# Performance work log

Hardware: AMD Instinct MI355X
Metric: run time of the kernel (lower is better)

The kernel has to match this reference:

```python
import jax, jax.numpy as jnp
import numpy as np

IMAGE_W, IMAGE_H = 1024, 800
STRIDES = (8, 16, 32, 64, 128)
LEVEL_HW = ((100, 128), (50, 64), (25, 32), (13, 16), (7, 8))
TOP_N = 1000
MIN_SCORE = 0.01
NMS_THR = 0.6
MAX_DET = 100
NUM_CLASSES = 80
BATCH = 16


def _grid(h, w, stride, b):
    ys = (jnp.arange(h, dtype=jnp.float32) + 0.5) * stride
    xs = (jnp.arange(w, dtype=jnp.float32) + 0.5) * stride
    gx, gy = jnp.meshgrid(xs, ys)  # [h, w]
    pos = jnp.stack([gx, gy], axis=-1)  # [h, w, 2] = (x, y)
    return jnp.broadcast_to(pos, (b, h, w, 2))


def setup_inputs() -> dict:
    key = jax.random.key(0)
    inp = {}
    for i, ((h, w), s) in enumerate(zip(LEVEL_HW, STRIDES)):
        key, k1, k2, k3 = jax.random.split(key, 4)
        inp[f"cls{i}"] = jax.random.normal(k1, (BATCH, h, w, NUM_CLASSES), jnp.float32)
        # +3 so exp(reg) gives realistic ~20px box extents
        inp[f"reg{i}"] = jax.random.normal(k2, (BATCH, h, w, 4), jnp.float32) + 3.0
        inp[f"ctr{i}"] = jax.random.normal(k3, (BATCH, h, w, 1), jnp.float32)
        inp[f"pos{i}"] = _grid(h, w, s, BATCH)
    return inp


def _level_filter(cls, reg, ctr, pos):
    b = cls.shape[0]
    cls = jax.nn.sigmoid(cls).reshape(b, -1, NUM_CLASSES)
    reg = jnp.exp(reg).reshape(b, -1, 4)
    ctr = jax.nn.sigmoid(ctr).reshape(b, -1)
    pos = pos.reshape(b, -1, 2)
    scores = jnp.sqrt(jnp.max(cls, axis=2) * ctr)  # [b, n]
    classes = jnp.argmax(cls, axis=2)  # [b, n] int
    if scores.shape[1] >= TOP_N:
        scores, idx = jax.lax.top_k(scores, TOP_N)
        classes = jnp.take_along_axis(classes, idx, axis=1)
        reg = jnp.take_along_axis(reg, idx[..., None], axis=1)
        pos = jnp.take_along_axis(pos, idx[..., None], axis=1)
        cls = jnp.take_along_axis(cls, idx[..., None], axis=1)
    return scores, classes, reg, pos, cls


def _decode_boxes(reg, pos):
    # ltrb offsets -> x1y1x2y2, truncate to int (torch .int()), clamp to image
    xy_min = pos - reg[..., 0:2]
    xy_max = pos + reg[..., 2:4]
    bx = jnp.trunc(jnp.concatenate([xy_min, xy_max], axis=-1))
    x1 = jnp.maximum(bx[..., 0], 0.0)
    y1 = jnp.maximum(bx[..., 1], 0.0)
    x2 = jnp.minimum(bx[..., 2], IMAGE_W - 1.0)
    y2 = jnp.minimum(bx[..., 3], IMAGE_H - 1.0)
    return jnp.stack([x1, y1, x2, y2], axis=-1)


def _nms_image(scores, classes, boxes, clsp):
    valid = scores > MIN_SCORE
    order = jnp.argsort(jnp.where(valid, -scores, jnp.inf))  # valid, desc score first
    s = scores[order]
    c = classes[order].astype(jnp.float32)
    b = boxes[order]
    cp = clsp[order]
    v = valid[order]
    # pairwise IoU (keep/suppress decisions are not differentiated)
    bb = jax.lax.stop_gradient(b)
    area = (bb[:, 2] - bb[:, 0]) * (bb[:, 3] - bb[:, 1])
    lt = jnp.maximum(bb[:, None, :2], bb[None, :, :2])
    rb = jnp.minimum(bb[:, None, 2:], bb[None, :, 2:])
    wh = jnp.maximum(rb - lt, 0.0)
    inter = wh[..., 0] * wh[..., 1]
    iou = inter / (area[:, None] + area[None, :] - inter)
    n = s.shape[0]
    idxs = jnp.arange(n)

    def body(i, keep):
        sup = keep[i] & (iou[i] > NMS_THR) & (idxs > i)
        return keep & ~sup

    keep = jax.lax.fori_loop(0, n, body, v)
    rank = jnp.cumsum(keep) - 1
    slot = jnp.where(keep & (rank < MAX_DET), rank, MAX_DET)  # MAX_DET -> dropped
    out_s = jnp.full((MAX_DET,), -1.0, jnp.float32).at[slot].set(s, mode="drop")
    out_c = jnp.full((MAX_DET,), -1.0, jnp.float32).at[slot].set(c, mode="drop")
    out_b = jnp.full((MAX_DET, 4), -1.0, jnp.float32).at[slot].set(b, mode="drop")
    out_cp = jnp.full((MAX_DET, NUM_CLASSES), -1.0, jnp.float32).at[slot].set(cp, mode="drop")
    return out_s, out_c, out_b, out_cp


def reference(cls0, cls1, cls2, cls3, cls4, reg0, reg1, reg2, reg3, reg4,
              ctr0, ctr1, ctr2, ctr3, ctr4, pos0, pos1, pos2, pos3, pos4):
    clss = [cls0, cls1, cls2, cls3, cls4]
    regs = [reg0, reg1, reg2, reg3, reg4]
    ctrs = [ctr0, ctr1, ctr2, ctr3, ctr4]
    poss = [pos0, pos1, pos2, pos3, pos4]
    parts = [_level_filter(c, r, t, p) for c, r, t, p in zip(clss, regs, ctrs, poss)]
    scores = jnp.concatenate([p[0] for p in parts], axis=1)
    classes = jnp.concatenate([p[1] for p in parts], axis=1)
    reg = jnp.concatenate([p[2] for p in parts], axis=1)
    pos = jnp.concatenate([p[3] for p in parts], axis=1)
    clsp = jnp.concatenate([p[4] for p in parts], axis=1)
    boxes = _decode_boxes(reg, pos)
    return jax.vmap(_nms_image)(scores, classes, boxes, clsp)
```

## Files before the change

### kernel.cpp

```cpp
#include <hip/hip_runtime.h>
#include <math.h>

#define TOTAL_G 17064
#define BATCHN  16
#define ALLF    0xFFFFFFFFFFFFFFFFull
#define INVALID_HI 0xC3DC28F5u

typedef unsigned long long u64;
typedef unsigned int u32;
typedef unsigned short u16;

#define KEYS0_OFF   0
#define KEYS1_OFF   1638400
#define KEYS234_OFF 2048000
#define CLSI_OFF    2187264
#define NC_OFF      2733312
#define T512_OFF    2733824
#define KR_OFF      2733952
#define MSK_OFF     2799488
#define SLOTK_OFF   3323776

struct Ptrs {
  const float *cls0,*cls1,*cls2,*cls3,*cls4;
  const float *reg0,*reg1,*reg2,*reg3,*reg4;
  const float *ctr0,*ctr1,*ctr2,*ctr3,*ctr4;
  const float *pos0,*pos1,*pos2,*pos3,*pos4;
  char *ws;
};

__device__ __forceinline__ float sigd(float x) {
  return (float)(1.0 / (1.0 + exp(-(double)x)));
}
__device__ __forceinline__ float dexp(float x) {
  return (float)exp((double)x);
}
__device__ __forceinline__ void levinfo(int gid, int& lev, int& idx, int& nl) {
  if      (gid < 12800) { lev=0; idx=gid;        nl=12800; }
  else if (gid < 16000) { lev=1; idx=gid-12800;  nl=3200;  }
  else if (gid < 16800) { lev=2; idx=gid-16000;  nl=800;   }
  else if (gid < 17008) { lev=3; idx=gid-16800;  nl=208;   }
  else                  { lev=4; idx=gid-17008;  nl=56;    }
}

__device__ __forceinline__ u64* krank_of(char* ws, int b) {
  return (u64*)(ws + KR_OFF + (size_t)b * 4096);
}
__device__ __forceinline__ u64* msk_of(char* ws, int b) {
  return (u64*)(ws + MSK_OFF + (size_t)b * 32768);
}
__device__ __forceinline__ u64* slotkey_of(char* ws, int b) {
  return (u64*)(ws + SLOTK_OFF + (size_t)b * 800);
}

__device__ __forceinline__ float4 decode_box(const Ptrs& P, int b, int gid) {
  int lev, idx, nl; levinfo(gid, lev, idx, nl);
  const float *rp, *pp;
  if      (lev == 0) { rp = P.reg0; pp = P.pos0; }
  else if (lev == 1) { rp = P.reg1; pp = P.pos1; }
  else if (lev == 2) { rp = P.reg2; pp = P.pos2; }
  else if (lev == 3) { rp = P.reg3; pp = P.pos3; }
  else               { rp = P.reg4; pp = P.pos4; }
  float4 rv = *(const float4*)(rp + (size_t)(b * nl + idx) * 4);
  float2 pv = *(const float2*)(pp + (size_t)(b * nl + idx) * 2);
  float e0 = dexp(rv.x), e1 = dexp(rv.y), e2 = dexp(rv.z), e3 = dexp(rv.w);
  float x1 = truncf(pv.x - e0), y1 = truncf(pv.y - e1);
  float x2 = truncf(pv.x + e2), y2 = truncf(pv.y + e3);
  x1 = fmaxf(x1, 0.0f); y1 = fmaxf(y1, 0.0f);
  x2 = fminf(x2, 1023.0f); y2 = fminf(y2, 799.0f);
  return make_float4(x1, y1, x2, y2);
}

__global__ __launch_bounds__(256) void k_score(Ptrs P) {
  __shared__ float4 sk4[64 * 20];
  int b = blockIdx.y;
  int tid = threadIdx.x;
  int p0 = blockIdx.x * 64;

  #pragma unroll
  for (int it = 0; it < 5; ++it) {
    int t4 = it * 256 + tid;
    int g = p0 + t4 / 20;
    if (g < TOTAL_G) {
      int sub = t4 - (t4 / 20) * 20;
      int lev, idx, nl; levinfo(g, lev, idx, nl);
      const float* clsb;
      if      (lev == 0) clsb = P.cls0;
      else if (lev == 1) clsb = P.cls1;
      else if (lev == 2) clsb = P.cls2;
      else if (lev == 3) clsb = P.cls3;
      else               clsb = P.cls4;
      sk4[t4] = ((const float4*)(clsb + (size_t)(b * nl + idx) * 80))[sub];
    }
  }
  __syncthreads();

  int lp = tid >> 2, q = tid & 3;
  int g = p0 + lp;
  if (g >= TOTAL_G) return;

  const float4* my4 = &sk4[lp * 20 + q * 5];
  float m = -INFINITY, m2 = -INFINITY; int mi = 0;
  #pragma unroll
  for (int k = 0; k < 5; ++k) {
    float4 v = my4[k];
    int base = q * 20 + 4 * k;
    if (v.x > m) { m2 = m; m = v.x; mi = base+0; } else if (v.x > m2) m2 = v.x;
    if (v.y > m) { m2 = m; m = v.y; mi = base+1; } else if (v.y > m2) m2 = v.y;
    if (v.z > m) { m2 = m; m = v.z; mi = base+2; } else if (v.z > m2) m2 = v.z;
    if (v.w > m) { m2 = m; m = v.w; mi = base+3; } else if (v.w > m2) m2 = v.w;
  }
  #pragma unroll
  for (int xw = 1; xw <= 2; xw <<= 1) {
    float om  = __shfl_xor(m,  xw);
    float om2 = __shfl_xor(m2, xw);
    int   omi = __shfl_xor(mi, xw);
    bool take = (om > m) || (om == m && omi < mi);
    float lm  = take ? m : om;
    float wm2 = take ? om2 : m2;
    if (take) { m = om; mi = omi; }
    m2 = fmaxf(lm, wm2);
  }

  float thr = fminf(m - 1e-3f, 9.0f);
  float pmax; int ci;
  if (m2 >= thr) {
    float pv = -1.0f; int pi = 0x7fffffff;
    #pragma unroll 1
    for (int k = 0; k < 5; ++k) {
      float4 v = my4[k];
      float xs[4] = {v.x, v.y, v.z, v.w};
      #pragma unroll
      for (int e = 0; e < 4; ++e) {
        if (xs[e] >= thr) {
          float p = sigd(xs[e]);
          if (p > pv) { pv = p; pi = q * 20 + 4 * k + e; }
        }
      }
    }
    #pragma unroll
    for (int xw = 1; xw <= 2; xw <<= 1) {
      float ov = __shfl_xor(pv, xw);
      int   oi = __shfl_xor(pi, xw);
      if (ov > pv || (ov == pv && oi < pi)) { pv = ov; pi = oi; }
    }
    pmax = pv; ci = pi;
  } else {
    pmax = sigd(m); ci = mi;
  }

  if (q == 0) {
    int lev, idx, nl; levinfo(g, lev, idx, nl);
    const float* ctrb;
    if      (lev == 0) ctrb = P.ctr0;
    else if (lev == 1) ctrb = P.ctr1;
    else if (lev == 2) ctrb = P.ctr2;
    else if (lev == 3) ctrb = P.ctr3;
    else               ctrb = P.ctr4;
    float tc = ctrb[(size_t)b * nl + idx];
    float csig = sigd(tc);
    float prod = pmax * csig;
    float s = (float)sqrt((double)prod);
    ((u16*)(P.ws + CLSI_OFF))[(size_t)b * TOTAL_G + g] = (u16)ci;
    unsigned hi = ~__float_as_uint(s);
    u64 key = ((u64)hi << 15) | (unsigned)g;
    if      (lev == 0) ((u64*)(P.ws + KEYS0_OFF))  [(size_t)b * 12800 + idx] = key;
    else if (lev == 1) ((u64*)(P.ws + KEYS1_OFF))  [(size_t)b * 3200  + idx] = key;
    else               ((u64*)(P.ws + KEYS234_OFF))[(size_t)b * 1088  + (g - 16000)] = key;
  }
}

struct SelSh {
  u32 hist[4][4096];
  u64 buf[64];
  u64 res, pfx;
  int t, mode, cnt;
};

__device__ __forceinline__ u64 loadkey(const Ptrs& P, int b, int u) {
  if (u < 12800) return ((const u64*)(P.ws + KEYS0_OFF))  [(size_t)b * 12800 + u];
  if (u < 16000) return ((const u64*)(P.ws + KEYS1_OFF))  [(size_t)b * 3200  + (u - 12800)];
  return               ((const u64*)(P.ws + KEYS234_OFF))[(size_t)b * 1088  + (u - 16000)];
}
__device__ __forceinline__ bool keep_pred(u64 k, int u, u64 T0, u64 T1) {
  bool valid = (u32)(k >> 15) < INVALID_HI;
  bool sel = (u < 12800) ? (k <= T0) : ((u < 16000) ? (k <= T1) : true);
  return valid && sel;
}

__device__ u64 fast_select(const Ptrs& P, int b, int pred, int t0, SelSh* S) {
  int tid = threadIdx.x, wid = tid >> 6, lane = tid & 63;
  int rep = wid & 3;
  u64 Pfx = 3; int t = t0;
  const int SS[4] = {33, 21, 9, 0};
  const int WW[4] = {12, 12, 12, 9};
  #pragma unroll 1
  for (int p = 0; p < 4; ++p) {
    int s = SS[p], wb = WW[p];
    u32 dmask = (1u << wb) - 1u;
    for (int i = tid; i < 4 * 4096; i += 1024) (&S->hist[0][0])[i] = 0;
    if (tid == 0) { S->mode = 0; S->cnt = 0; }
    __syncthreads();
    for (int i = tid; i < TOTAL_G; i += 1024) {
      u64 k = loadkey(P, b, i);
      if (pred == 2 && !((u32)(k >> 15) < INVALID_HI)) continue;
      if ((k >> (s + wb)) == Pfx)
        atomicAdd(&S->hist[rep][(u32)(k >> s) & dmask], 1u);
    }
    __syncthreads();
    for (int i = tid; i < 4096; i += 1024) {
      u32 v = S->hist[0][i] + S->hist[1][i] + S->hist[2][i] + S->hist[3][i];
      S->hist[0][i] = v;
    }
    __syncthreads();
    if (wid == 0) {
      u32 ssum = 0;
      #pragma unroll 8
      for (int i = 0; i < 64; ++i) {
        int ii = (i + lane) & 63;
        ssum += S->hist[0][(lane << 6) + ii];
      }
      u32 inc = ssum;
      for (int o = 1; o < 64; o <<= 1) { u32 v = __shfl_up(inc, o); if (lane >= o) inc += v; }
      u64 ball = __ballot(inc >= (u32)t);
      if (!ball) {
        if (lane == 0) { S->mode = 9; S->res = ALLF; }
      } else {
        int Wq = __ffsll(ball) - 1;
        u32 cumBefore = __shfl(inc - ssum, Wq);
        u32 v2 = S->hist[0][(Wq << 6) + lane];
        u32 inc2 = v2;
        for (int o = 1; o < 64; o <<= 1) { u32 x = __shfl_up(inc2, o); if (lane >= o) inc2 += x; }
        u64 ball2 = __ballot(cumBefore + inc2 >= (u32)t);
        int l2 = __ffsll(ball2) - 1;
        u32 cumB2 = __shfl(cumBefore + inc2 - v2, l2);
        u32 c = __shfl(v2, l2);
        if (lane == 0) {
          int d = (Wq << 6) + l2;
          u64 np = (Pfx << wb) | (u32)d;
          S->pfx = np; S->t = t - (int)cumB2;
          if (s == 0)       { S->mode = 9; S->res = np; }
          else if (c == 1)  { S->mode = 1; }
          else if (c <= 64) { S->mode = 2; }
        }
      }
    }
    __syncthreads();
    int mode = S->mode; u64 np = S->pfx; int tt = S->t;
    if (mode == 9) return S->res;
    if (mode == 1 || mode == 2) {
      for (int i = tid; i < TOTAL_G; i += 1024) {
        u64 k = loadkey(P, b, i);
        if (pred == 2 && !((u32)(k >> 15) < INVALID_HI)) continue;
        if ((k >> s) == np) {
          if (mode == 1) S->res = k;
          else { int pos = atomicAdd(&S->cnt, 1); S->buf[pos] = k; }
        }
      }
      __syncthreads();
      if (mode == 2 && wid == 0) {
        int c2 = S->cnt;
        u64 kl = (lane < c2) ? S->buf[lane] : ALLF;
        int r = 0;
        for (int j = 0; j < c2; ++j) r += (S->buf[j] < kl) ? 1 : 0;
        if (lane < c2 && r == tt - 1) S->res = kl;
      }
      __syncthreads();
      return S->res;
    }
    Pfx = np; t = tt;
    __syncthreads();
  }
  return S->pfx;
}

__global__ __launch_bounds__(1024) void k_mask(Ptrs P) {
  __shared__ union USh {
    SelSh S;
    struct { float4 sbox[512]; u64 smaskR[4096]; u16 parts[1024]; } M;
  } U;
  __shared__ u64 skey[512];
  __shared__ u16 srank[512];
  __shared__ int wbase[272];
  __shared__ int sN5;
  int qi = blockIdx.x, b = blockIdx.y;
  int tid = threadIdx.x, wid = tid >> 6, lane = tid & 63;
  char* ws = P.ws;

  u64 T512 = fast_select(P, b, 2, 512, &U.S);
  if (qi == 0 && tid == 0) ((u64*)(ws + T512_OFF))[b] = T512;

  for (int it = 0; it < 17; ++it) {
    int u = it * 1024 + tid;
    bool keep5 = false;
    if (u < TOTAL_G) {
      u64 k = loadkey(P, b, u);
      keep5 = ((u32)(k >> 15) < INVALID_HI) && (k <= T512);
    }
    u64 bal = __ballot(keep5);
    if (lane == 0) wbase[it * 16 + wid] = __popcll(bal);
  }
  __syncthreads();
  if (wid == 0) {
    int carry = 0;
    for (int base = 0; base < 272; base += 64) {
      int idx = base + lane;
      int v = (idx < 272) ? wbase[idx] : 0;
      int inc = v;
      for (int o = 1; o < 64; o <<= 1) { int x = __shfl_up(inc, o); if (lane >= o) inc += x; }
      if (idx < 272) wbase[idx] = inc - v + carry;
      carry += __shfl(inc, 63);
    }
    if (lane == 0) sN5 = carry;
  }
  __syncthreads();
  int n512 = sN5;
  if (qi == 0 && tid == 0) ((int*)(ws + NC_OFF))[16 + b] = n512;

  for (int it = 0; it < 17; ++it) {
    int u = it * 1024 + tid;
    bool keep5 = false; u64 k = 0;
    if (u < TOTAL_G) {
      k = loadkey(P, b, u);
      keep5 = ((u32)(k >> 15) < INVALID_HI) && (k <= T512);
    }
    u64 bal = __ballot(keep5);
    int pos = wbase[it * 16 + wid] + __popcll(bal & ((1ull << lane) - 1ull));
    if (keep5) skey[pos] = k;
  }
  __syncthreads();

  if (tid < 512) {
    if (tid < n512) {
      U.M.sbox[tid] = decode_box(P, b, (int)(skey[tid] & 0x7FFF));
    } else {
      skey[tid] = (ALLF - 511) + (u64)tid;
      U.M.sbox[tid] = make_float4(-1e30f, -1e30f, -1e30f, -1e30f);
    }
  }
  for (int i = tid; i < 512 * 8; i += 1024) U.M.smaskR[i] = 0ull;
  __syncthreads();

  {
    int t2 = tid & 511, half = tid >> 9;
    u64 mykey = skey[t2];
    int jb = half << 8, cnt = 0;
    #pragma unroll 4
    for (int j = jb; j < jb + 256; ++j) cnt += (skey[j] < mykey) ? 1 : 0;
    U.M.parts[tid] = (u16)cnt;
  }
  __syncthreads();
  if (tid < 512) srank[tid] = (u16)(U.M.parts[tid] + U.M.parts[tid + 512]);
  __syncthreads();

  int i = qi * 128 + (tid >> 3);
  int w = tid & 7;
  float4 bi = U.M.sbox[i];
  u64 ki = skey[i];
  int ri = srank[i];
  float ia = (bi.z - bi.x) * (bi.w - bi.y);
  #pragma unroll 8
  for (int bj = 0; bj < 64; ++bj) {
    int jj = (bj + w) & 63;
    int j = (w << 6) | jj;
    u64 kj = skey[j];
    if (ki < kj) {
      float4 bj4 = U.M.sbox[j];
      float ja  = (bj4.z - bj4.x) * (bj4.w - bj4.y);
      float ltx = fmaxf(bi.x, bj4.x), lty = fmaxf(bi.y, bj4.y);
      float rbx = fminf(bi.z, bj4.z), rby = fminf(bi.w, bj4.w);
      float wv = fmaxf(rbx - ltx, 0.0f), hv = fmaxf(rby - lty, 0.0f);
      float inter = wv * hv;
      float iou = inter / (ia + ja - inter);
      if (iou > 0.6f) {
        int rj = srank[j];
        atomicOr(&U.M.smaskR[ri * 8 + (rj >> 6)], 1ull << (rj & 63));
      }
    }
  }
  __syncthreads();

  {
    int il = tid >> 3, ww = tid & 7;
    int ig = qi * 128 + il;
    if (ig < n512) {
      int r = srank[ig];
      msk_of(ws, b)[r * 8 + ww] = U.M.smaskR[r * 8 + ww];
      if (ww == 0) krank_of(ws, b)[r] = skey[ig];
    }
  }
}

__device__ u64 select256(const u64* keys, int n, int t0, u32* hist, u64* shP, int* shT) {
  u64 Pfx = 3; int t = t0;
  const int SS[4] = {33, 21, 9, 0};
  const int WW[4] = {12, 12, 12, 9};
  for (int p = 0; p < 4; ++p) {
    int s = SS[p], wb = WW[p];
    u32 dmask = (1u << wb) - 1u;
    for (int i = threadIdx.x; i < 4096; i += 256) hist[i] = 0;
    __syncthreads();
    for (int i = threadIdx.x; i < n; i += 256) {
      u64 k = keys[i];
      if ((k >> (s + wb)) == Pfx) atomicAdd(&hist[(u32)(k >> s) & dmask], 1u);
    }
    __syncthreads();
    if (threadIdx.x < 64) {
      int lane = threadIdx.x;
      u32 ssum = 0;
      for (int i = 0; i < 64; ++i) ssum += hist[(lane << 6) + ((i + lane) & 63)];
      u32 inc = ssum;
      for (int o = 1; o < 64; o <<= 1) { u32 v = __shfl_up(inc, o); if (lane >= o) inc += v; }
      u64 ball = __ballot(inc >= (u32)t);
      int Wq = __ffsll(ball) - 1;
      u32 cumBefore = __shfl(inc - ssum, Wq);
      u32 v2 = hist[(Wq << 6) + lane];
      u32 inc2 = v2;
      for (int o = 1; o < 64; o <<= 1) { u32 x = __shfl_up(inc2, o); if (lane >= o) inc2 += x; }
      u64 ball2 = __ballot(cumBefore + inc2 >= (u32)t);
      int l2 = __ffsll(ball2) - 1;
      u32 cumB2 = __shfl(cumBefore + inc2 - v2, l2);
      if (lane == 0) { *shP = (Pfx << wb) | (u32)((Wq << 6) + l2); *shT = t - (int)cumB2; }
    }
    __syncthreads();
    Pfx = *shP; t = *shT;
    __syncthreads();
  }
  return Pfx;
}

__global__ __launch_bounds__(256) void k_reduce(Ptrs P) {
  __shared__ u64 smask[4096];
  __shared__ u32 keeplist[100];
  __shared__ int keptS;
  __shared__ u64 liveC[267];
  __shared__ union UF {
    u32 hist[4096];
    struct { u64 pk[256]; int pc[256]; float4 fkb[100]; } F;
  } UF_;
  __shared__ u64 shP; __shared__ int shT;
  __shared__ u64 bk; __shared__ int bc2;

  int b = blockIdx.x;
  int tid = threadIdx.x;
  char* ws = P.ws;
  int n512 = ((int*)(ws + NC_OFF))[16 + b];
  const u64* kr = krank_of(ws, b);

  const u64* gmask = msk_of(ws, b);
  for (int t = tid; t < 4096; t += 256) smask[t] = gmask[t];
  __syncthreads();

  if (tid < 64) {
    int lane = tid;
    u64 lw = 0;
    if (lane < 8) {
      int lo = lane << 6;
      int c = n512 - lo; if (c < 0) c = 0; if (c > 64) c = 64;
      lw = (c >= 64) ? ALLF : ((c > 0) ? ((1ull << c) - 1ull) : 0ull);
    }
    int kept = 0;
    while (kept < 100) {
      bool nz = (lane < 8) && (lw != 0ull);
      u64 bal = __ballot(nz);
      if (!bal) break;
      int W = __ffsll(bal) - 1;
      u64 wv = __shfl(lw, W);
      int bit = __ffsll(wv) - 1;
      int i = (W << 6) + bit;
      if (lane == 0) keeplist[kept] = (u32)i;
      kept++;
      if (lane == W) lw &= ~(1ull << bit);
      if (kept == 100) break;
      if (lane < 8) lw &= ~smask[i * 8 + lane];
    }
    if (lane == 0) keptS = kept;
  }
  __syncthreads();
  int kept = keptS;
  int keptW = kept;

  if (kept < 100 && n512 == 512) {
    u64 T0 = select256((const u64*)(ws + KEYS0_OFF) + (size_t)b * 12800, 12800, 1000,
                       UF_.hist, &shP, &shT);
    u64 T1 = select256((const u64*)(ws + KEYS1_OFF) + (size_t)b * 3200, 3200, 1000,
                       UF_.hist, &shP, &shT);
    u64 T512 = ((u64*)(ws + T512_OFF))[b];
    for (int w = tid; w < 267; w += 256) {
      int lo = w << 6;
      u64 m = 0;
      for (int e = 0; e < 64; ++e) {
        int u = lo + e;
        if (u < TOTAL_G) {
          u64 k = loadkey(P, b, u);
          if (keep_pred(k, u, T0, T1) && k > T512) m |= (1ull << e);
        }
      }
      liveC[w] = m;
    }
    if (tid < kept) UF_.F.fkb[tid] = decode_box(P, b, (int)(kr[keeplist[tid]] & 0x7FFF));
    __syncthreads();

    for (int k2 = 0; k2 < kept; ++k2) {
      float4 bi = UF_.F.fkb[k2];
      float ia = (bi.z - bi.x) * (bi.w - bi.y);
      for (int u = tid; u < TOTAL_G; u += 256) {
        if (!((liveC[u >> 6] >> (u & 63)) & 1ull)) continue;
        float4 bj4 = decode_box(P, b, u);
        float ja  = (bj4.z - bj4.x) * (bj4.w - bj4.y);
        float ltx = fmaxf(bi.x, bj4.x), lty = fmaxf(bi.y, bj4.y);
        float rbx = fminf(bi.z, bj4.z), rby = fminf(bi.w, bj4.w);
        float wv = fmaxf(rbx - ltx, 0.0f), hv = fmaxf(rby - lty, 0.0f);
        float inter = wv * hv;
        float iou = inter / (ia + ja - inter);
        if (iou > 0.6f) atomicAnd(&liveC[u >> 6], ~(1ull << (u & 63)));
      }
    }
    __syncthreads();

    while (kept < 100) {
      u64 mymin = ALLF; int myc = -1;
      for (int u = tid; u < TOTAL_G; u += 256) {
        if (!((liveC[u >> 6] >> (u & 63)) & 1ull)) continue;
        u64 k = loadkey(P, b, u);
        if (k < mymin) { mymin = k; myc = u; }
      }
      UF_.F.pk[tid] = mymin; UF_.F.pc[tid] = myc;
      __syncthreads();
      if (tid < 64) {
        u64 m = UF_.F.pk[tid]; int c0 = UF_.F.pc[tid];
        #pragma unroll
        for (int o = 64; o < 256; o += 64)
          if (UF_.F.pk[tid + o] < m) { m = UF_.F.pk[tid + o]; c0 = UF_.F.pc[tid + o]; }
        for (int o = 32; o > 0; o >>= 1) {
          u64 om = __shfl_down(m, o); int oc = __shfl_down(c0, o);
          if (om < m) { m = om; c0 = oc; }
        }
        if (tid == 0) { bk = m; bc2 = c0; }
      }
      __syncthreads();
      if (bk == ALLF) break;
      int cs = bc2;
      if (tid == 0) {
        slotkey_of(ws, b)[kept] = bk;
        atomicAnd(&liveC[cs >> 6], ~(1ull << (cs & 63)));
      }
      __syncthreads();
      kept++;
      if (kept == 100) break;
      float4 bi = decode_box(P, b, cs);
      float ia = (bi.z - bi.x) * (bi.w - bi.y);
      for (int u = tid; u < TOTAL_G; u += 256) {
        if (!((liveC[u >> 6] >> (u & 63)) & 1ull)) continue;
        float4 bj4 = decode_box(P, b, u);
        float ja  = (bj4.z - bj4.x) * (bj4.w - bj4.y);
        float ltx = fmaxf(bi.x, bj4.x), lty = fmaxf(bi.y, bj4.y);
        float rbx = fminf(bi.z, bj4.z), rby = fminf(bi.w, bj4.w);
        float wv = fmaxf(rbx - ltx, 0.0f), hv = fmaxf(rby - lty, 0.0f);
        float inter = wv * hv;
        float iou = inter / (ia + ja - inter);
        if (iou > 0.6f) atomicAnd(&liveC[u >> 6], ~(1ull << (u & 63)));
      }
      __syncthreads();
    }
  }

  if (tid < 100) {
    if (tid < keptW)      slotkey_of(ws, b)[tid] = kr[keeplist[tid]];
    else if (tid >= kept) slotkey_of(ws, b)[tid] = ALLF;
  }
}

__global__ __launch_bounds__(256) void k_out(Ptrs P, float* out) {
  int b = blockIdx.x, part = blockIdx.y;
  int s0 = part * 10;
  int tid = threadIdx.x;
  const u64* skl = slotkey_of(P.ws, b);

  if (tid < 10) {
    int s = s0 + tid;
    u64 key = skl[s];
    float os = -1.0f, oc = -1.0f;
    float4 bx = make_float4(-1.0f, -1.0f, -1.0f, -1.0f);
    if (key != ALLF) {
      int gid = (int)(key & 0x7FFF);
      os = __uint_as_float(~(u32)(key >> 15));
      oc = (float)((u16*)(P.ws + CLSI_OFF))[(size_t)b * TOTAL_G + gid];
      bx = decode_box(P, b, gid);
    }
    out[b * 100 + s] = os;
    out[1600 + b * 100 + s] = oc;
    *(float4*)(out + 3200 + (size_t)(b * 100 + s) * 4) = bx;
  }

  for (int t = tid; t < 800; t += 256) {
    int sl = t / 80, k = t - sl * 80;
    int s = s0 + sl;
    u64 key = skl[s];
    float val = -1.0f;
    if (key != ALLF) {
      int gid = (int)(key & 0x7FFF);
      int lev, idx, nl; levinfo(gid, lev, idx, nl);
      const float* cp;
      if      (lev == 0) cp = P.cls0;
      else if (lev == 1) cp = P.cls1;
      else if (lev == 2) cp = P.cls2;
      else if (lev == 3) cp = P.cls3;
      else               cp = P.cls4;
      val = sigd(cp[(size_t)(b * nl + idx) * 80 + k]);
    }
    out[9600 + (size_t)(b * 100 + s) * 80 + k] = val;
  }
}

extern "C" void kernel_launch(void* const* d_in, const int* in_sizes, int n_in,
                              void* d_out, int out_size, void* d_ws, size_t ws_size,
                              hipStream_t stream) {
  (void)in_sizes; (void)n_in; (void)out_size; (void)ws_size;
  Ptrs P;
  P.cls0 = (const float*)d_in[0];  P.reg0 = (const float*)d_in[1];
  P.ctr0 = (const float*)d_in[2];  P.pos0 = (const float*)d_in[3];
  P.cls1 = (const float*)d_in[4];  P.reg1 = (const float*)d_in[5];
  P.ctr1 = (const float*)d_in[6];  P.pos1 = (const float*)d_in[7];
  P.cls2 = (const float*)d_in[8];  P.reg2 = (const float*)d_in[9];
  P.ctr2 = (const float*)d_in[10]; P.pos2 = (const float*)d_in[11];
  P.cls3 = (const float*)d_in[12]; P.reg3 = (const float*)d_in[13];
  P.ctr3 = (const float*)d_in[14]; P.pos3 = (const float*)d_in[15];
  P.cls4 = (const float*)d_in[16]; P.reg4 = (const float*)d_in[17];
  P.ctr4 = (const float*)d_in[18]; P.pos4 = (const float*)d_in[19];
  P.ws = (char*)d_ws;

  k_score<<<dim3(267, 16), 256, 0, stream>>>(P);
  k_mask<<<dim3(4, 16), 1024, 0, stream>>>(P);
  k_reduce<<<16, 256, 0, stream>>>(P);
  k_out<<<dim3(16, 10), 256, 0, stream>>>(P, (float*)d_out);
}
```

Before: 109.3 us.

## Replace exact multi-pass top-512 radix select with single-pass bucket boundary

Drops the exact four-pass radix select that found the 512th-best key. It now builds one 12-bit histogram over the key's high bits and keeps every candidate strictly below the bucket that crosses 512, so the on-chip candidate set holds at most 512 keys and usually slightly fewer. The stored threshold becomes boundary minus one, and the fallback path now runs whenever fewer than 100 boxes survive, no longer only when exactly 512 candidates existed. This removes up to three extra histogram passes over all keys per block, at the cost of possibly reaching the slower fallback path more often.

```diff
diff --git a/kernel.cpp b/kernel.cpp
--- a/kernel.cpp
+++ b/kernel.cpp
@@ -169,13 +169,6 @@
   }
 }
 
-struct SelSh {
-  u32 hist[4][4096];
-  u64 buf[64];
-  u64 res, pfx;
-  int t, mode, cnt;
-};
-
 __device__ __forceinline__ u64 loadkey(const Ptrs& P, int b, int u) {
   if (u < 12800) return ((const u64*)(P.ws + KEYS0_OFF))  [(size_t)b * 12800 + u];
   if (u < 16000) return ((const u64*)(P.ws + KEYS1_OFF))  [(size_t)b * 3200  + (u - 12800)];
@@ -187,114 +180,69 @@
   return valid && sel;
 }
 
-__device__ u64 fast_select(const Ptrs& P, int b, int pred, int t0, SelSh* S) {
-  int tid = threadIdx.x, wid = tid >> 6, lane = tid & 63;
-  int rep = wid & 3;
-  u64 Pfx = 3; int t = t0;
-  const int SS[4] = {33, 21, 9, 0};
-  const int WW[4] = {12, 12, 12, 9};
-  #pragma unroll 1
-  for (int p = 0; p < 4; ++p) {
-    int s = SS[p], wb = WW[p];
-    u32 dmask = (1u << wb) - 1u;
-    for (int i = tid; i < 4 * 4096; i += 1024) (&S->hist[0][0])[i] = 0;
-    if (tid == 0) { S->mode = 0; S->cnt = 0; }
-    __syncthreads();
-    for (int i = tid; i < TOTAL_G; i += 1024) {
-      u64 k = loadkey(P, b, i);
-      if (pred == 2 && !((u32)(k >> 15) < INVALID_HI)) continue;
-      if ((k >> (s + wb)) == Pfx)
-        atomicAdd(&S->hist[rep][(u32)(k >> s) & dmask], 1u);
-    }
-    __syncthreads();
-    for (int i = tid; i < 4096; i += 1024) {
-      u32 v = S->hist[0][i] + S->hist[1][i] + S->hist[2][i] + S->hist[3][i];
-      S->hist[0][i] = v;
-    }
-    __syncthreads();
-    if (wid == 0) {
-      u32 ssum = 0;
-      #pragma unroll 8
-      for (int i = 0; i < 64; ++i) {
-        int ii = (i + lane) & 63;
-        ssum += S->hist[0][(lane << 6) + ii];
-      }
-      u32 inc = ssum;
-      for (int o = 1; o < 64; o <<= 1) { u32 v = __shfl_up(inc, o); if (lane >= o) inc += v; }
-      u64 ball = __ballot(inc >= (u32)t);
-      if (!ball) {
-        if (lane == 0) { S->mode = 9; S->res = ALLF; }
-      } else {
-        int Wq = __ffsll(ball) - 1;
-        u32 cumBefore = __shfl(inc - ssum, Wq);
-        u32 v2 = S->hist[0][(Wq << 6) + lane];
-        u32 inc2 = v2;
-        for (int o = 1; o < 64; o <<= 1) { u32 x = __shfl_up(inc2, o); if (lane >= o) inc2 += x; }
-        u64 ball2 = __ballot(cumBefore + inc2 >= (u32)t);
-        int l2 = __ffsll(ball2) - 1;
-        u32 cumB2 = __shfl(cumBefore + inc2 - v2, l2);
-        u32 c = __shfl(v2, l2);
-        if (lane == 0) {
-          int d = (Wq << 6) + l2;
-          u64 np = (Pfx << wb) | (u32)d;
-          S->pfx = np; S->t = t - (int)cumB2;
-          if (s == 0)       { S->mode = 9; S->res = np; }
-          else if (c == 1)  { S->mode = 1; }
-          else if (c <= 64) { S->mode = 2; }
-        }
-      }
-    }
-    __syncthreads();
-    int mode = S->mode; u64 np = S->pfx; int tt = S->t;
-    if (mode == 9) return S->res;
-    if (mode == 1 || mode == 2) {
-      for (int i = tid; i < TOTAL_G; i += 1024) {
-        u64 k = loadkey(P, b, i);
-        if (pred == 2 && !((u32)(k >> 15) < INVALID_HI)) continue;
-        if ((k >> s) == np) {
-          if (mode == 1) S->res = k;
-          else { int pos = atomicAdd(&S->cnt, 1); S->buf[pos] = k; }
-        }
-      }
-      __syncthreads();
-      if (mode == 2 && wid == 0) {
-        int c2 = S->cnt;
-        u64 kl = (lane < c2) ? S->buf[lane] : ALLF;
-        int r = 0;
-        for (int j = 0; j < c2; ++j) r += (S->buf[j] < kl) ? 1 : 0;
-        if (lane < c2 && r == tt - 1) S->res = kl;
-      }
-      __syncthreads();
-      return S->res;
-    }
-    Pfx = np; t = tt;
-    __syncthreads();
-  }
-  return S->pfx;
-}
-
 __global__ __launch_bounds__(1024) void k_mask(Ptrs P) {
   __shared__ union USh {
-    SelSh S;
+    u32 H[4][4096];
     struct { float4 sbox[512]; u64 smaskR[4096]; u16 parts[1024]; } M;
   } U;
   __shared__ u64 skey[512];
   __shared__ u16 srank[512];
   __shared__ int wbase[272];
   __shared__ int sN5;
+  __shared__ u64 sBoundary;
   int qi = blockIdx.x, b = blockIdx.y;
   int tid = threadIdx.x, wid = tid >> 6, lane = tid & 63;
   char* ws = P.ws;
 
-  u64 T512 = fast_select(P, b, 2, 512, &U.S);
-  if (qi == 0 && tid == 0) ((u64*)(ws + T512_OFF))[b] = T512;
+  for (int i = tid; i < 4 * 4096; i += 1024) (&U.H[0][0])[i] = 0;
+  __syncthreads();
+  for (int u = tid; u < TOTAL_G; u += 1024) {
+    u64 k = loadkey(P, b, u);
+    if ((u32)(k >> 15) < INVALID_HI)
+      atomicAdd(&U.H[wid & 3][(u32)(k >> 29) & 0xFFF], 1u);
+  }
+  __syncthreads();
+  for (int i = tid; i < 4096; i += 1024) {
+    u32 v = U.H[0][i] + U.H[1][i] + U.H[2][i] + U.H[3][i];
+    U.H[0][i] = v;
+  }
+  __syncthreads();
+  if (wid == 0) {
+    u32 ssum = 0;
+    #pragma unroll 8
+    for (int i = 0; i < 64; ++i) {
+      int ii = (i + lane) & 63;
+      ssum += U.H[0][(lane << 6) + ii];
+    }
+    u32 inc = ssum;
+    for (int o = 1; o < 64; o <<= 1) { u32 v = __shfl_up(inc, o); if (lane >= o) inc += v; }
+    u64 ball = __ballot(inc >= 512u);
+    if (!ball) {
+      if (lane == 0) sBoundary = ((u64)INVALID_HI << 15);
+    } else {
+      int Wq = __ffsll(ball) - 1;
+      u32 cumBefore = __shfl(inc - ssum, Wq);
+      u32 v2 = U.H[0][(Wq << 6) + lane];
+      u32 inc2 = v2;
+      for (int o = 1; o < 64; o <<= 1) { u32 x = __shfl_up(inc2, o); if (lane >= o) inc2 += x; }
+      u64 ball2 = __ballot(cumBefore + inc2 >= 512u);
+      int l2 = __ffsll(ball2) - 1;
+      if (lane == 0) {
+        int d = (Wq << 6) + l2;
+        sBoundary = (48ull << 41) | ((u64)d << 29);
+      }
+    }
+  }
+  __syncthreads();
+  u64 Boundary = sBoundary;
+  if (qi == 0 && tid == 0) ((u64*)(ws + T512_OFF))[b] = Boundary - 1;
 
   for (int it = 0; it < 17; ++it) {
     int u = it * 1024 + tid;
     bool keep5 = false;
     if (u < TOTAL_G) {
       u64 k = loadkey(P, b, u);
-      keep5 = ((u32)(k >> 15) < INVALID_HI) && (k <= T512);
+      keep5 = ((u32)(k >> 15) < INVALID_HI) && (k < Boundary);
     }
     u64 bal = __ballot(keep5);
     if (lane == 0) wbase[it * 16 + wid] = __popcll(bal);
@@ -321,7 +269,7 @@
     bool keep5 = false; u64 k = 0;
     if (u < TOTAL_G) {
       k = loadkey(P, b, u);
-      keep5 = ((u32)(k >> 15) < INVALID_HI) && (k <= T512);
+      keep5 = ((u32)(k >> 15) < INVALID_HI) && (k < Boundary);
     }
     u64 bal = __ballot(keep5);
     int pos = wbase[it * 16 + wid] + __popcll(bal & ((1ull << lane) - 1ull));
@@ -479,7 +427,7 @@
   int kept = keptS;
   int keptW = kept;
 
-  if (kept < 100 && n512 == 512) {
+  if (kept < 100) {
     u64 T0 = select256((const u64*)(ws + KEYS0_OFF) + (size_t)b * 12800, 12800, 1000,
                        UF_.hist, &shP, &shT);
     u64 T1 = select256((const u64*)(ws + KEYS1_OFF) + (size_t)b * 3200, 3200, 1000,
```

Result: faster. 99.13 us (-9.3%).
